# Performance work log

Measured on AMD Instinct MI355X. Metric: run time of the kernel, lower is better.

The kernel has to match this reference:

```python
import jax, jax.numpy as jnp
import numpy as np

HEADS, POINTS = 8, 4
EPS = 1e-5
BS, C, H, W = 2, 256, 200, 200


def _layernorm(x, g, b):
    m = x.mean(-1, keepdims=True)
    v = ((x - m) ** 2).mean(-1, keepdims=True)
    return (x - m) / jnp.sqrt(v + EPS) * g + b


def _sine_pos(bs, Hh, Ww, num_feats, temperature=10000.0):
    # mmdet SinePositionalEncoding with all-zeros mask: cumsum of ones -> 1..H / 1..W
    y = jnp.arange(1, Hh + 1, dtype=jnp.float32)
    x = jnp.arange(1, Ww + 1, dtype=jnp.float32)
    dim_t = jnp.arange(num_feats, dtype=jnp.float32)
    dim_t = temperature ** (2.0 * jnp.floor(dim_t / 2.0) / num_feats)

    def interleave(p):  # p: [N, num_feats] -> [sin(p0),cos(p1),sin(p2),...]
        return jnp.stack((jnp.sin(p[:, 0::2]), jnp.cos(p[:, 1::2])), axis=-1).reshape(p.shape[0], -1)

    pos_x = interleave(x[:, None] / dim_t)  # [W, nf]
    pos_y = interleave(y[:, None] / dim_t)  # [H, nf]
    pos = jnp.concatenate([
        jnp.broadcast_to(pos_y[:, None, :], (Hh, Ww, num_feats)),
        jnp.broadcast_to(pos_x[None, :, :], (Hh, Ww, num_feats)),
    ], axis=-1)  # [H, W, 2*nf] (channel order matches cat((pos_y,pos_x),dim=1) after flatten/permute)
    return jnp.broadcast_to(pos.reshape(1, Hh * Ww, 2 * num_feats), (bs, Hh * Ww, 2 * num_feats))


def _bilinear_sample(v, x, y):
    # v: [bs, heads, H, W, hd]; x, y: [bs, heads, N] pixel coords (align_corners=False, zero padding)
    bs, nh, Hh, Ww, hd = v.shape
    vf = v.reshape(bs, nh, Hh * Ww, hd)
    x0 = jnp.floor(x)
    y0 = jnp.floor(y)
    wx = x - x0
    wy = y - y0

    def gather(xi, yi):
        valid = (xi >= 0) & (xi < Ww) & (yi >= 0) & (yi < Hh)
        xc = jnp.clip(xi, 0, Ww - 1).astype(jnp.int32)
        yc = jnp.clip(yi, 0, Hh - 1).astype(jnp.int32)
        idx = yc * Ww + xc
        g = jnp.take_along_axis(vf, idx[..., None], axis=2)  # [bs, nh, N, hd]
        return g * valid[..., None].astype(v.dtype)

    out = gather(x0, y0) * ((1 - wx) * (1 - wy))[..., None]
    out = out + gather(x0 + 1, y0) * (wx * (1 - wy))[..., None]
    out = out + gather(x0, y0 + 1) * ((1 - wx) * wy)[..., None]
    out = out + gather(x0 + 1, y0 + 1) * (wx * wy)[..., None]
    return out


def _dfa_layer(out, ref, pos, Hh, Ww, p):
    bs, Lq, Cc = out.shape
    hd = Cc // HEADS
    q = out + pos
    value = out @ p['vp_w'].T + p['vp_b']  # [bs, Lq, C]
    off = (q @ p['off_w'].T + p['off_b']).reshape(bs, Lq, HEADS, POINTS, 2)
    aw = jax.nn.softmax((q @ p['aw_w'].T + p['aw_b']).reshape(bs, Lq, HEADS, POINTS), axis=-1)
    norm = jnp.array([Ww, Hh], dtype=out.dtype)
    loc = ref[None, :, None, None, :] + off / norm  # [bs, Lq, heads, P, 2] normalized [0,1]
    x = loc[..., 0] * Ww - 0.5
    y = loc[..., 1] * Hh - 0.5
    v = value.reshape(bs, Lq, HEADS, hd).transpose(0, 2, 1, 3).reshape(bs, HEADS, Hh, Ww, hd)
    xt = x.transpose(0, 2, 1, 3).reshape(bs, HEADS, Lq * POINTS)
    yt = y.transpose(0, 2, 1, 3).reshape(bs, HEADS, Lq * POINTS)
    samp = _bilinear_sample(v, xt, yt).reshape(bs, HEADS, Lq, POINTS, hd)
    attn = jnp.einsum('bhqpd,bqhp->bqhd', samp, aw).reshape(bs, Lq, Cc)
    attn = attn @ p['op_w'].T + p['op_b']
    out = _layernorm(out + attn, p['ln1_g'], p['ln1_b'])
    ffn = jax.nn.relu(out @ p['l1_w'].T + p['l1_b']) @ p['l2_w'].T + p['l2_b']
    return _layernorm(out + ffn, p['ln2_g'], p['ln2_b'])


def setup_inputs() -> dict:
    key = jax.random.key(0)
    ks = jax.random.split(key, 20)
    s = 0.02
    L = 3
    return {
        'bev_feat': jax.random.normal(ks[0], (BS, C, H, W), jnp.float32),
        'proj_q_w': jax.random.normal(ks[1], (C, C), jnp.float32) * s,
        'proj_q_b': jax.random.normal(ks[2], (C,), jnp.float32) * s,
        'off_w': jax.random.normal(ks[3], (L, HEADS * POINTS * 2, C), jnp.float32) * s,
        'off_b': jax.random.normal(ks[4], (L, HEADS * POINTS * 2), jnp.float32) * s,
        'aw_w': jax.random.normal(ks[5], (L, HEADS * POINTS, C), jnp.float32) * s,
        'aw_b': jax.random.normal(ks[6], (L, HEADS * POINTS), jnp.float32) * s,
        'vp_w': jax.random.normal(ks[7], (L, C, C), jnp.float32) * s,
        'vp_b': jax.random.normal(ks[8], (L, C), jnp.float32) * s,
        'op_w': jax.random.normal(ks[9], (L, C, C), jnp.float32) * s,
        'op_b': jax.random.normal(ks[10], (L, C), jnp.float32) * s,
        'ln1_g': jnp.ones((L, C), jnp.float32),
        'ln1_b': jnp.zeros((L, C), jnp.float32),
        'l1_w': jax.random.normal(ks[11], (L, C, C), jnp.float32) * s,
        'l1_b': jax.random.normal(ks[12], (L, C), jnp.float32) * s,
        'l2_w': jax.random.normal(ks[13], (L, C, C), jnp.float32) * s,
        'l2_b': jax.random.normal(ks[14], (L, C), jnp.float32) * s,
        'ln2_g': jnp.ones((L, C), jnp.float32),
        'ln2_b': jnp.zeros((L, C), jnp.float32),
    }


def reference(bev_feat, proj_q_w, proj_q_b, off_w, off_b, aw_w, aw_b, vp_w, vp_b,
              op_w, op_b, ln1_g, ln1_b, l1_w, l1_b, l2_w, l2_b, ln2_g, ln2_b):
    bs, Cc, Hh, Ww = bev_feat.shape
    x = bev_feat.reshape(bs, Cc, Hh * Ww).transpose(0, 2, 1)  # [bs, HW, C]
    out = x @ proj_q_w.T + proj_q_b
    # reference points: pixel centers normalized to [0,1]
    ry, rx = jnp.meshgrid(jnp.linspace(0.5, Hh - 0.5, Hh) / Hh,
                          jnp.linspace(0.5, Ww - 0.5, Ww) / Ww, indexing='ij')
    ref = jnp.stack([rx.reshape(-1), ry.reshape(-1)], axis=-1).astype(bev_feat.dtype)  # [HW, 2]
    pos = _sine_pos(bs, Hh, Ww, Cc // 2).astype(bev_feat.dtype)
    n_layers = off_w.shape[0]
    for i in range(n_layers):
        p = dict(off_w=off_w[i], off_b=off_b[i], aw_w=aw_w[i], aw_b=aw_b[i],
                 vp_w=vp_w[i], vp_b=vp_b[i], op_w=op_w[i], op_b=op_b[i],
                 ln1_g=ln1_g[i], ln1_b=ln1_b[i], l1_w=l1_w[i], l1_b=l1_b[i],
                 l2_w=l2_w[i], l2_b=l2_b[i], ln2_g=ln2_g[i], ln2_b=ln2_b[i])
        out = _dfa_layer(out, ref, pos, Hh, Ww, p)
    return out.transpose(0, 2, 1).reshape(bs, Cc, Hh, Ww)
```

## Files before the change

kernel.cpp:

```cpp
#include <hip/hip_runtime.h>
#include <math.h>

#define HEADS 8
#define POINTS 4
#define BSZ 2
#define CDIM 256
#define HH 200
#define WW 200
#define LQ (HH * WW)
#define MTOT (BSZ * LQ)
#define NLAYERS 3
#define MPAD 40064

typedef __attribute__((ext_vector_type(8))) short shortx8;
typedef __attribute__((ext_vector_type(4))) float floatx4;

__device__ __forceinline__ ushort f2b(float f) {
    union { float f; unsigned u; } v; v.f = f;
    unsigned r = v.u + 0x7fffu + ((v.u >> 16) & 1u);
    return (ushort)(r >> 16);
}
__device__ __forceinline__ float b2f(ushort b) {
    union { unsigned u; float f; } v; v.u = ((unsigned)b) << 16;
    return v.f;
}
__device__ __forceinline__ float bitsf(unsigned u) {
    union { unsigned u; float f; } v; v.u = u;
    return v.f;
}
__device__ __forceinline__ uint packbf(float lo, float hi) {
    return (uint)f2b(lo) | ((uint)f2b(hi) << 16);
}

__device__ __forceinline__ int permc(int c) {
    return (c & ~63) | (((c & 15) << 2) | ((c & 63) >> 4));
}
__device__ __forceinline__ int iperm(int p) {
    return (p & ~63) | (((p & 3) << 4) | ((p & 63) >> 2));
}

__global__ __launch_bounds__(256)
void cvt_kernel(const float* __restrict__ in, ushort* __restrict__ out)
{
    const int i = (blockIdx.x * 256 + threadIdx.x) * 4;
    const float4 v = *(const float4*)(in + i);
    ushort4 o;
    o.x = f2b(v.x); o.y = f2b(v.y); o.z = f2b(v.z); o.w = f2b(v.w);
    *(ushort4*)(out + i) = o;
}

__global__ __launch_bounds__(256)
void cvt_perm_kernel(const float* __restrict__ in, ushort* __restrict__ out)
{
    const int idx = (blockIdx.x * 256 + threadIdx.x) * 4;
    const int rowb = idx & ~255;
    const int p0 = idx & 255;
    ushort4 o;
    o.x = f2b(in[rowb + iperm(p0 + 0)]);
    o.y = f2b(in[rowb + iperm(p0 + 1)]);
    o.z = f2b(in[rowb + iperm(p0 + 2)]);
    o.w = f2b(in[rowb + iperm(p0 + 3)]);
    *(ushort4*)(out + idx) = o;
}

__global__ __launch_bounds__(256)
void build_offaw(const float* __restrict__ offw, const float* __restrict__ offb,
                 const float* __restrict__ aww, const float* __restrict__ awb,
                 ushort* __restrict__ wout, float* __restrict__ bout)
{
    const int blk = blockIdx.x;
    const int i = blk >> 7;
    const int r = blk & 127;
    const int c = threadIdx.x;
    float v = 0.f;
    if (r < 64)      v = offw[((size_t)i * 64 + r) * CDIM + c];
    else if (r < 96) v = aww[((size_t)i * 32 + (r - 64)) * CDIM + c];
    wout[((size_t)i * 128 + r) * CDIM + permc(c)] = f2b(v);
    if (c == 0) {
        float bb = 0.f;
        if (r < 64)      bb = offb[i * 64 + r];
        else if (r < 96) bb = awb[i * 32 + (r - 64)];
        bout[i * 128 + r] = bb;
    }
}

__global__ __launch_bounds__(256)
void pos_kernel(ushort* __restrict__ pos)
{
    const int idx = blockIdx.x * 256 + threadIdx.x;
    const int c = idx & 255;
    const int l = idx >> 8;
    const int cc = c & 127;
    const float coord = (c < 128) ? (float)(l / WW + 1) : (float)(l % WW + 1);
    const float expo = (float)(2 * (cc >> 1)) * (1.0f / 128.0f);
    const float t = powf(10000.0f, expo);
    const float ph = coord / t;
    pos[(size_t)l * CDIM + permc(c)] = f2b((cc & 1) ? cosf(ph) : sinf(ph));
}

__global__ __launch_bounds__(256)
void bevT_kernel(const float* __restrict__ in, ushort* __restrict__ out)
{
    __shared__ float tile[32][33];
    const int b = blockIdx.z;
    const int l0 = blockIdx.x * 32;
    const int c0 = blockIdx.y * 32;
    const float* ib = in + (size_t)b * CDIM * LQ;
    ushort* ob = out + (size_t)b * LQ * CDIM;
    #pragma unroll
    for (int j = 0; j < 32; j += 8)
        tile[threadIdx.y + j][threadIdx.x] =
            ib[(size_t)(c0 + threadIdx.y + j) * LQ + l0 + threadIdx.x];
    __syncthreads();
    #pragma unroll
    for (int j = 0; j < 32; j += 8)
        ob[(size_t)(l0 + threadIdx.y + j) * CDIM + c0 + threadIdx.x] =
            f2b(tile[threadIdx.x][threadIdx.y + j]);
}

#define LSTR 40

template<bool RELU, bool F32OUT, bool BF16OUT, bool ROWADD>
__global__ __launch_bounds__(256)
void mfma_gemm(const ushort* __restrict__ A, const ushort* __restrict__ B,
               const float* __restrict__ bias,
               float* __restrict__ Cf, ushort* __restrict__ Cb,
               const ushort* __restrict__ rowtab,
               int N, int K)
{
    __shared__ ushort As[128 * LSTR];
    __shared__ ushort Bs[128 * LSTR];
    const int tid = threadIdx.x;
    const int lane = tid & 63;
    const int wave = tid >> 6;
    const int wr = (wave >> 1) * 64;
    const int wc = (wave & 1) * 64;
    const int rowBase = blockIdx.y * 128;
    const int colBase = blockIdx.x * 128;

    floatx4 acc[4][4];
    #pragma unroll
    for (int i = 0; i < 4; i++)
        #pragma unroll
        for (int j = 0; j < 4; j++) {
            floatx4 z = {0.f, 0.f, 0.f, 0.f};
            acc[i][j] = z;
        }

    const int strow = tid >> 2;
    const int stcol = (tid & 3) * 8;
    const int kq = (lane >> 4) * 8;
    const int lr = lane & 15;

    for (int k0 = 0; k0 < K; k0 += 32) {
        #pragma unroll
        for (int j = 0; j < 2; j++) {
            const int r = j * 64 + strow;
            const uint4 av = *(const uint4*)(A + (size_t)(rowBase + r) * K + k0 + stcol);
            const uint4 bv = *(const uint4*)(B + (size_t)(colBase + r) * K + k0 + stcol);
            *(uint4*)(As + r * LSTR + stcol) = av;
            *(uint4*)(Bs + r * LSTR + stcol) = bv;
        }
        __syncthreads();
        shortx8 af[4], bfr[4];
        #pragma unroll
        for (int t = 0; t < 4; t++) {
            af[t]  = *(const shortx8*)(As + (wr + t * 16 + lr) * LSTR + kq);
            bfr[t] = *(const shortx8*)(Bs + (wc + t * 16 + lr) * LSTR + kq);
        }
        #pragma unroll
        for (int mt = 0; mt < 4; mt++)
            #pragma unroll
            for (int nt = 0; nt < 4; nt++)
                acc[mt][nt] = __builtin_amdgcn_mfma_f32_16x16x32_bf16(
                    af[mt], bfr[nt], acc[mt][nt], 0, 0, 0);
        __syncthreads();
    }

    const int colB = colBase + wc + lr;
    const int rowB = rowBase + wr + (lane >> 4) * 4;
    #pragma unroll
    for (int mt = 0; mt < 4; mt++) {
        #pragma unroll
        for (int r = 0; r < 4; r++) {
            const int m = rowB + mt * 16 + r;
            const int pr = (m >= LQ) ? m - LQ : m;
            #pragma unroll
            for (int nt = 0; nt < 4; nt++) {
                const int n = colB + nt * 16;
                float v = acc[mt][nt][r];
                if (ROWADD) v += b2f(rowtab[(size_t)pr * 384 + n]);
                else        v += bias[n];
                if (RELU) v = fmaxf(v, 0.f);
                if (F32OUT) Cf[(size_t)m * N + n] = v;
                if (BF16OUT) Cb[(size_t)m * N + n] = f2b(v);
            }
        }
    }
}

template<bool RELU, bool F32OUT, bool BF16OUT, bool PERMC>
__global__ __launch_bounds__(512, 1)
void gemm_fused(const ushort* __restrict__ A, const ushort* __restrict__ B,
                const float* __restrict__ bias,
                float* __restrict__ resid, ushort* __restrict__ Cb)
{
    __shared__ ushort As[2][128 * LSTR];
    __shared__ ushort Bs[2][256 * LSTR];

    const int tid = threadIdx.x;
    const int lane = tid & 63;
    const int wave = tid >> 6;
    const int lr = lane & 15;
    const int hi = lane >> 4;
    const int rowBase = blockIdx.x * 128;
    const int wr = (wave >> 2) * 64;
    const int wc = (wave & 3) * 64;

    floatx4 acc[4][4];
    #pragma unroll
    for (int i = 0; i < 4; i++)
        #pragma unroll
        for (int j = 0; j < 4; j++) {
            floatx4 z = {0.f, 0.f, 0.f, 0.f};
            acc[i][j] = z;
        }

    const int strow = tid >> 2;
    const int stcol = (tid & 3) * 8;
    const int kq = hi * 8;

    const ushort* ag = A + (size_t)(rowBase + strow) * CDIM + stcol;
    const ushort* bg = B + (size_t)strow * CDIM + stcol;

    {
        const uint4 av  = *(const uint4*)(ag);
        const uint4 bv0 = *(const uint4*)(bg);
        const uint4 bv1 = *(const uint4*)(bg + 128 * CDIM);
        *(uint4*)(As[0] + strow * LSTR + stcol) = av;
        *(uint4*)(Bs[0] + strow * LSTR + stcol) = bv0;
        *(uint4*)(Bs[0] + (strow + 128) * LSTR + stcol) = bv1;
    }

    #pragma unroll
    for (int kt = 0; kt < 8; ++kt) {
        const int p = kt & 1;
        __syncthreads();
        uint4 av, bv0, bv1;
        if (kt < 7) {
            const int ko = (kt + 1) * 32;
            av  = *(const uint4*)(ag + ko);
            bv0 = *(const uint4*)(bg + ko);
            bv1 = *(const uint4*)(bg + ko + 128 * CDIM);
        }
        shortx8 af[4], bfr[4];
        #pragma unroll
        for (int t = 0; t < 4; t++) {
            af[t]  = *(const shortx8*)(As[p] + (wr + t * 16 + lr) * LSTR + kq);
            bfr[t] = *(const shortx8*)(Bs[p] + (wc + t * 16 + lr) * LSTR + kq);
        }
        #pragma unroll
        for (int mt = 0; mt < 4; mt++)
            #pragma unroll
            for (int nt = 0; nt < 4; nt++)
                acc[mt][nt] = __builtin_amdgcn_mfma_f32_16x16x32_bf16(
                    af[mt], bfr[nt], acc[mt][nt], 0, 0, 0);
        if (kt < 7) {
            *(uint4*)(As[p ^ 1] + strow * LSTR + stcol) = av;
            *(uint4*)(Bs[p ^ 1] + strow * LSTR + stcol) = bv0;
            *(uint4*)(Bs[p ^ 1] + (strow + 128) * LSTR + stcol) = bv1;
        }
    }

    float bcol[4];
    #pragma unroll
    for (int nt = 0; nt < 4; nt++) bcol[nt] = bias[wc + nt * 16 + lr];

    #pragma unroll
    for (int mt = 0; mt < 4; mt++) {
        #pragma unroll
        for (int r = 0; r < 4; r++) {
            const int m = rowBase + wr + mt * 16 + hi * 4 + r;
            float4 wv;
            ushort4 ob;
            #pragma unroll
            for (int nt = 0; nt < 4; nt++) {
                float y = acc[mt][nt][r] + bcol[nt];
                if (RELU) y = fmaxf(y, 0.f);
                (&wv.x)[nt] = y;
                if (PERMC) {
                    if (BF16OUT) (&ob.x)[nt] = f2b(y);
                } else {
                    const int col = wc + nt * 16 + lr;
                    if (BF16OUT) Cb[(size_t)m * CDIM + col] = f2b(y);
                }
            }
            if (F32OUT) *(float4*)(resid + (size_t)m * CDIM + wc + lr * 4) = wv;
            if (PERMC && BF16OUT)
                *(ushort4*)(Cb + (size_t)m * CDIM + wc + lr * 4) = ob;
        }
    }
}

#define LSTR2 36
#define LSTR3 264

template<bool BF16OUT>
__global__ __launch_bounds__(256, 1)
void ffn_fused(const ushort* __restrict__ attn, const ushort* __restrict__ Wop,
               const float* __restrict__ opb,
               const ushort* __restrict__ Wl1, const float* __restrict__ l1b,
               const ushort* __restrict__ Wl2, const float* __restrict__ l2b,
               float* __restrict__ resid, ushort* __restrict__ outb,
               const float* __restrict__ g1, const float* __restrict__ b1,
               const float* __restrict__ g2, const float* __restrict__ b2)
{
    __shared__ ushort As[2][64 * LSTR2];
    __shared__ ushort Bs[2][256 * LSTR2];
    __shared__ ushort Ls[64 * LSTR3];

    const int tid = threadIdx.x;
    const int lane = tid & 63;
    const int wave = tid >> 6;
    const int lr = lane & 15;
    const int hi = lane >> 4;
    const int rowBase = blockIdx.x * 64;
    const int wc = wave * 64;

    const int strow = tid >> 2;
    const int stcol = (tid & 3) * 8;
    const int kq = hi * 8;

    floatx4 acc1[4][4];
    #pragma unroll
    for (int i = 0; i < 4; i++)
        #pragma unroll
        for (int j = 0; j < 4; j++) {
            floatx4 z = {0.f, 0.f, 0.f, 0.f};
            acc1[i][j] = z;
        }

    {
        const ushort* ag = attn + (size_t)(rowBase + strow) * CDIM + stcol;
        const ushort* bg = Wop + (size_t)strow * CDIM + stcol;
        {
            const uint4 av  = *(const uint4*)(ag);
            const uint4 bv0 = *(const uint4*)(bg);
            const uint4 bv1 = *(const uint4*)(bg + 64 * CDIM);
            const uint4 bv2 = *(const uint4*)(bg + 128 * CDIM);
            const uint4 bv3 = *(const uint4*)(bg + 192 * CDIM);
            *(uint4*)(As[0] + strow * LSTR2 + stcol) = av;
            *(uint4*)(Bs[0] + strow * LSTR2 + stcol) = bv0;
            *(uint4*)(Bs[0] + (strow + 64) * LSTR2 + stcol) = bv1;
            *(uint4*)(Bs[0] + (strow + 128) * LSTR2 + stcol) = bv2;
            *(uint4*)(Bs[0] + (strow + 192) * LSTR2 + stcol) = bv3;
        }
        #pragma unroll
        for (int kt = 0; kt < 8; ++kt) {
            const int p = kt & 1;
            __syncthreads();
            uint4 av, bv0, bv1, bv2, bv3;
            if (kt < 7) {
                const int ko = (kt + 1) * 32;
                av  = *(const uint4*)(ag + ko);
                bv0 = *(const uint4*)(bg + ko);
                bv1 = *(const uint4*)(bg + ko + 64 * CDIM);
                bv2 = *(const uint4*)(bg + ko + 128 * CDIM);
                bv3 = *(const uint4*)(bg + ko + 192 * CDIM);
            }
            shortx8 af[4], bfr[4];
            #pragma unroll
            for (int t = 0; t < 4; t++) {
                af[t]  = *(const shortx8*)(As[p] + (t * 16 + lr) * LSTR2 + kq);
                bfr[t] = *(const shortx8*)(Bs[p] + (wc + t * 16 + lr) * LSTR2 + kq);
            }
            #pragma unroll
            for (int mt = 0; mt < 4; mt++)
                #pragma unroll
                for (int nt = 0; nt < 4; nt++)
                    acc1[mt][nt] = __builtin_amdgcn_mfma_f32_16x16x32_bf16(
                        af[mt], bfr[nt], acc1[mt][nt], 0, 0, 0);
            if (kt < 7) {
                *(uint4*)(As[p ^ 1] + strow * LSTR2 + stcol) = av;
                *(uint4*)(Bs[p ^ 1] + strow * LSTR2 + stcol) = bv0;
                *(uint4*)(Bs[p ^ 1] + (strow + 64) * LSTR2 + stcol) = bv1;
                *(uint4*)(Bs[p ^ 1] + (strow + 128) * LSTR2 + stcol) = bv2;
                *(uint4*)(Bs[p ^ 1] + (strow + 192) * LSTR2 + stcol) = bv3;
            }
        }
        __syncthreads();
    }

    {
        float bcol[4];
        #pragma unroll
        for (int nt = 0; nt < 4; nt++) bcol[nt] = opb[wc + nt * 16 + lr];
        float2 (*red)[4] = (float2(*)[4])As[0];
        #pragma unroll
        for (int mt = 0; mt < 4; mt++) {
            #pragma unroll
            for (int r = 0; r < 4; r++) {
                const int mrel = mt * 16 + hi * 4 + r;
                const int m = rowBase + mrel;
                const float4 rv = *(const float4*)(resid + (size_t)m * CDIM + wc + lr * 4);
                float s = 0.f, sq = 0.f;
                #pragma unroll
                for (int nt = 0; nt < 4; nt++) {
                    float x = acc1[mt][nt][r] + bcol[nt] + (&rv.x)[nt];
                    acc1[mt][nt][r] = x;
                    s += x; sq += x * x;
                }
                #pragma unroll
                for (int o = 8; o >= 1; o >>= 1) {
                    s  += __shfl_xor(s, o, 64);
                    sq += __shfl_xor(sq, o, 64);
                }
                if (lr == 0) { float2 t2; t2.x = s; t2.y = sq; red[mrel][wave] = t2; }
            }
        }
        __syncthreads();
        float gcol[4], btcol[4];
        #pragma unroll
        for (int nt = 0; nt < 4; nt++) {
            gcol[nt]  = g1[wc + nt * 16 + lr];
            btcol[nt] = b1[wc + nt * 16 + lr];
        }
        #pragma unroll
        for (int mt = 0; mt < 4; mt++) {
            #pragma unroll
            for (int r = 0; r < 4; r++) {
                const int mrel = mt * 16 + hi * 4 + r;
                const float2 t0 = red[mrel][0], t1 = red[mrel][1];
                const float2 t2 = red[mrel][2], t3 = red[mrel][3];
                const float S  = (t0.x + t1.x) + (t2.x + t3.x);
                const float SQ = (t0.y + t1.y) + (t2.y + t3.y);
                const float mean = S * (1.0f / CDIM);
                const float var = SQ * (1.0f / CDIM) - mean * mean;
                const float rstd = rsqrtf(var + 1e-5f);
                ushort4 yb;
                #pragma unroll
                for (int nt = 0; nt < 4; nt++) {
                    const float y = (acc1[mt][nt][r] - mean) * rstd * gcol[nt] + btcol[nt];
                    acc1[mt][nt][r] = y;
                    (&yb.x)[nt] = f2b(y);
                }
                *(ushort4*)(Ls + mrel * LSTR3 + wc + lr * 4) = yb;
            }
        }
    }

    floatx4 acc2[4][4];
    #pragma unroll
    for (int i = 0; i < 4; i++)
        #pragma unroll
        for (int j = 0; j < 4; j++) {
            floatx4 z = {0.f, 0.f, 0.f, 0.f};
            acc2[i][j] = z;
        }
    {
        const ushort* bg = Wl1 + (size_t)strow * CDIM + stcol;
        {
            const uint4 bv0 = *(const uint4*)(bg);
            const uint4 bv1 = *(const uint4*)(bg + 64 * CDIM);
            const uint4 bv2 = *(const uint4*)(bg + 128 * CDIM);
            const uint4 bv3 = *(const uint4*)(bg + 192 * CDIM);
            *(uint4*)(Bs[0] + strow * LSTR2 + stcol) = bv0;
            *(uint4*)(Bs[0] + (strow + 64) * LSTR2 + stcol) = bv1;
            *(uint4*)(Bs[0] + (strow + 128) * LSTR2 + stcol) = bv2;
            *(uint4*)(Bs[0] + (strow + 192) * LSTR2 + stcol) = bv3;
        }
        #pragma unroll
        for (int kt = 0; kt < 8; ++kt) {
            const int p = kt & 1;
            __syncthreads();
            uint4 bv0, bv1, bv2, bv3;
            if (kt < 7) {
                const int ko = (kt + 1) * 32;
                bv0 = *(const uint4*)(bg + ko);
                bv1 = *(const uint4*)(bg + ko + 64 * CDIM);
                bv2 = *(const uint4*)(bg + ko + 128 * CDIM);
                bv3 = *(const uint4*)(bg + ko + 192 * CDIM);
            }
            shortx8 af[4], bfr[4];
            #pragma unroll
            for (int t = 0; t < 4; t++) {
                af[t]  = *(const shortx8*)(Ls + (t * 16 + lr) * LSTR3 + kt * 32 + kq);
                bfr[t] = *(const shortx8*)(Bs[p] + (wc + t * 16 + lr) * LSTR2 + kq);
            }
            #pragma unroll
            for (int mt = 0; mt < 4; mt++)
                #pragma unroll
                for (int nt = 0; nt < 4; nt++)
                    acc2[mt][nt] = __builtin_amdgcn_mfma_f32_16x16x32_bf16(
                        af[mt], bfr[nt], acc2[mt][nt], 0, 0, 0);
            if (kt < 7) {
                *(uint4*)(Bs[p ^ 1] + strow * LSTR2 + stcol) = bv0;
                *(uint4*)(Bs[p ^ 1] + (strow + 64) * LSTR2 + stcol) = bv1;
                *(uint4*)(Bs[p ^ 1] + (strow + 128) * LSTR2 + stcol) = bv2;
                *(uint4*)(Bs[p ^ 1] + (strow + 192) * LSTR2 + stcol) = bv3;
            }
        }
        __syncthreads();
        float bcol2[4];
        #pragma unroll
        for (int nt = 0; nt < 4; nt++) bcol2[nt] = l1b[wc + nt * 16 + lr];
        #pragma unroll
        for (int mt = 0; mt < 4; mt++) {
            #pragma unroll
            for (int r = 0; r < 4; r++) {
                const int mrel = mt * 16 + hi * 4 + r;
                ushort4 hb;
                #pragma unroll
                for (int nt = 0; nt < 4; nt++)
                    (&hb.x)[nt] = f2b(fmaxf(acc2[mt][nt][r] + bcol2[nt], 0.f));
                *(ushort4*)(Ls + mrel * LSTR3 + wc + lr * 4) = hb;
            }
        }
    }

    #pragma unroll
    for (int i = 0; i < 4; i++)
        #pragma unroll
        for (int j = 0; j < 4; j++) {
            floatx4 z = {0.f, 0.f, 0.f, 0.f};
            acc2[i][j] = z;
        }
    {
        const ushort* bg = Wl2 + (size_t)strow * CDIM + stcol;
        {
            const uint4 bv0 = *(const uint4*)(bg);
            const uint4 bv1 = *(const uint4*)(bg + 64 * CDIM);
            const uint4 bv2 = *(const uint4*)(bg + 128 * CDIM);
            const uint4 bv3 = *(const uint4*)(bg + 192 * CDIM);
            *(uint4*)(Bs[0] + strow * LSTR2 + stcol) = bv0;
            *(uint4*)(Bs[0] + (strow + 64) * LSTR2 + stcol) = bv1;
            *(uint4*)(Bs[0] + (strow + 128) * LSTR2 + stcol) = bv2;
            *(uint4*)(Bs[0] + (strow + 192) * LSTR2 + stcol) = bv3;
        }
        #pragma unroll
        for (int kt = 0; kt < 8; ++kt) {
            const int p = kt & 1;
            __syncthreads();
            uint4 bv0, bv1, bv2, bv3;
            if (kt < 7) {
                const int ko = (kt + 1) * 32;
                bv0 = *(const uint4*)(bg + ko);
                bv1 = *(const uint4*)(bg + ko + 64 * CDIM);
                bv2 = *(const uint4*)(bg + ko + 128 * CDIM);
                bv3 = *(const uint4*)(bg + ko + 192 * CDIM);
            }
            shortx8 af[4], bfr[4];
            #pragma unroll
            for (int t = 0; t < 4; t++) {
                af[t]  = *(const shortx8*)(Ls + (t * 16 + lr) * LSTR3 + kt * 32 + kq);
                bfr[t] = *(const shortx8*)(Bs[p] + (wc + t * 16 + lr) * LSTR2 + kq);
            }
            #pragma unroll
            for (int mt = 0; mt < 4; mt++)
                #pragma unroll
                for (int nt = 0; nt < 4; nt++)
                    acc2[mt][nt] = __builtin_amdgcn_mfma_f32_16x16x32_bf16(
                        af[mt], bfr[nt], acc2[mt][nt], 0, 0, 0);
            if (kt < 7) {
                *(uint4*)(Bs[p ^ 1] + strow * LSTR2 + stcol) = bv0;
                *(uint4*)(Bs[p ^ 1] + (strow + 64) * LSTR2 + stcol) = bv1;
                *(uint4*)(Bs[p ^ 1] + (strow + 128) * LSTR2 + stcol) = bv2;
                *(uint4*)(Bs[p ^ 1] + (strow + 192) * LSTR2 + stcol) = bv3;
            }
        }
        __syncthreads();
    }
    {
        float bcol3[4];
        #pragma unroll
        for (int nt = 0; nt < 4; nt++) bcol3[nt] = l2b[wc + nt * 16 + lr];
        float2 (*red)[4] = (float2(*)[4])As[0];
        #pragma unroll
        for (int mt = 0; mt < 4; mt++) {
            #pragma unroll
            for (int r = 0; r < 4; r++) {
                const int mrel = mt * 16 + hi * 4 + r;
                float s = 0.f, sq = 0.f;
                #pragma unroll
                for (int nt = 0; nt < 4; nt++) {
                    float x = acc2[mt][nt][r] + bcol3[nt] + acc1[mt][nt][r];
                    acc2[mt][nt][r] = x;
                    s += x; sq += x * x;
                }
                #pragma unroll
                for (int o = 8; o >= 1; o >>= 1) {
                    s  += __shfl_xor(s, o, 64);
                    sq += __shfl_xor(sq, o, 64);
                }
                if (lr == 0) { float2 t2; t2.x = s; t2.y = sq; red[mrel][wave] = t2; }
            }
        }
        __syncthreads();
        float gcol[4], btcol[4];
        #pragma unroll
        for (int nt = 0; nt < 4; nt++) {
            gcol[nt]  = g2[wc + nt * 16 + lr];
            btcol[nt] = b2[wc + nt * 16 + lr];
        }
        #pragma unroll
        for (int mt = 0; mt < 4; mt++) {
            #pragma unroll
            for (int r = 0; r < 4; r++) {
                const int mrel = mt * 16 + hi * 4 + r;
                const int m = rowBase + mrel;
                const float2 t0 = red[mrel][0], t1 = red[mrel][1];
                const float2 t2 = red[mrel][2], t3 = red[mrel][3];
                const float S  = (t0.x + t1.x) + (t2.x + t3.x);
                const float SQ = (t0.y + t1.y) + (t2.y + t3.y);
                const float mean = S * (1.0f / CDIM);
                const float var = SQ * (1.0f / CDIM) - mean * mean;
                const float rstd = rsqrtf(var + 1e-5f);
                float4 wv;
                ushort4 ob;
                #pragma unroll
                for (int nt = 0; nt < 4; nt++) {
                    const float y = (acc2[mt][nt][r] - mean) * rstd * gcol[nt] + btcol[nt];
                    (&wv.x)[nt] = y;
                    if (BF16OUT) (&ob.x)[nt] = f2b(y);
                }
                *(float4*)(resid + (size_t)m * CDIM + wc + lr * 4) = wv;
                if (BF16OUT) *(ushort4*)(outb + (size_t)m * CDIM + wc + lr * 4) = ob;
            }
        }
    }
}

__global__ __launch_bounds__(256)
void sample_kernel(const ushort* __restrict__ val,
                   const float* __restrict__ offaw,
                   ushort* __restrict__ attn)
{
    const int tid = threadIdx.x;
    const int m = blockIdx.x * 8 + (tid >> 5);
    const int lane = tid & 31;
    const int head = lane >> 2;
    const int c = head * 32 + (lane & 3) * 8;
    const int b = (m >= LQ) ? 1 : 0;
    const int l = m - (b ? LQ : 0);

    const float* row = offaw + (size_t)m * 128;
    const float4 lg  = *(const float4*)(row + 64 + head * 4);
    const float4 o01 = *(const float4*)(row + head * 8);
    const float4 o23 = *(const float4*)(row + head * 8 + 4);

    const float mx = fmaxf(fmaxf(lg.x, lg.y), fmaxf(lg.z, lg.w));
    const float e0 = expf(lg.x - mx), e1 = expf(lg.y - mx);
    const float e2 = expf(lg.z - mx), e3 = expf(lg.w - mx);
    const float inv = 1.0f / (e0 + e1 + e2 + e3);
    const float awv[4] = {e0 * inv, e1 * inv, e2 * inv, e3 * inv};

    const float lx = (float)(l % WW);
    const float ly = (float)(l / WW);
    const float px[4] = {lx + o01.x, lx + o01.z, lx + o23.x, lx + o23.z};
    const float py[4] = {ly + o01.y, ly + o01.w, ly + o23.y, ly + o23.w};

    const ushort* vb = val + (size_t)b * LQ * CDIM;
    uint4 cv[16];
    float cw[16];
    #pragma unroll
    for (int p = 0; p < POINTS; p++) {
        const float x = px[p], y = py[p];
        const float xf = floorf(x), yf = floorf(y);
        const int x0 = (int)xf, y0 = (int)yf;
        const float wx = x - xf, wy = y - yf;
        const int x0c = min(max(x0, 0), WW - 1);
        const int x1c = min(max(x0 + 1, 0), WW - 1);
        const int y0c = min(max(y0, 0), HH - 1);
        const int y1c = min(max(y0 + 1, 0), HH - 1);
        const float vx0 = (x0 >= 0 && x0 < WW) ? 1.f : 0.f;
        const float vx1 = (x0 + 1 >= 0 && x0 + 1 < WW) ? 1.f : 0.f;
        const float vy0 = (y0 >= 0 && y0 < HH) ? 1.f : 0.f;
        const float vy1 = (y0 + 1 >= 0 && y0 + 1 < HH) ? 1.f : 0.f;
        const float a = awv[p];
        cw[p * 4 + 0] = a * (1.f - wx) * (1.f - wy) * vx0 * vy0;
        cw[p * 4 + 1] = a * wx * (1.f - wy) * vx1 * vy0;
        cw[p * 4 + 2] = a * (1.f - wx) * wy * vx0 * vy1;
        cw[p * 4 + 3] = a * wx * wy * vx1 * vy1;
        const int r0 = y0c * WW, r1 = y1c * WW;
        cv[p * 4 + 0] = *(const uint4*)(vb + (((unsigned)(r0 + x0c)) << 8) + c);
        cv[p * 4 + 1] = *(const uint4*)(vb + (((unsigned)(r0 + x1c)) << 8) + c);
        cv[p * 4 + 2] = *(const uint4*)(vb + (((unsigned)(r1 + x0c)) << 8) + c);
        cv[p * 4 + 3] = *(const uint4*)(vb + (((unsigned)(r1 + x1c)) << 8) + c);
    }
    float a0 = 0.f, a1 = 0.f, a2 = 0.f, a3 = 0.f;
    float a4 = 0.f, a5 = 0.f, a6 = 0.f, a7 = 0.f;
    #pragma unroll
    for (int i = 0; i < 16; i++) {
        const float wgt = cw[i];
        a0 = fmaf(wgt, bitsf(cv[i].x << 16), a0);
        a1 = fmaf(wgt, bitsf(cv[i].x & 0xffff0000u), a1);
        a2 = fmaf(wgt, bitsf(cv[i].y << 16), a2);
        a3 = fmaf(wgt, bitsf(cv[i].y & 0xffff0000u), a3);
        a4 = fmaf(wgt, bitsf(cv[i].z << 16), a4);
        a5 = fmaf(wgt, bitsf(cv[i].z & 0xffff0000u), a5);
        a6 = fmaf(wgt, bitsf(cv[i].w << 16), a6);
        a7 = fmaf(wgt, bitsf(cv[i].w & 0xffff0000u), a7);
    }
    uint4 o;
    o.x = packbf(a0, a1); o.y = packbf(a2, a3);
    o.z = packbf(a4, a5); o.w = packbf(a6, a7);
    *(uint4*)(attn + (size_t)m * CDIM + c) = o;
}

__global__ __launch_bounds__(256)
void transpose_out(const float* __restrict__ in, float* __restrict__ outp)
{
    __shared__ float tile[32][33];
    const int b = blockIdx.z;
    const int l0 = blockIdx.x * 32;
    const int c0 = blockIdx.y * 32;
    const float* ib = in + (size_t)b * LQ * CDIM;
    float* ob = outp + (size_t)b * CDIM * LQ;
    #pragma unroll
    for (int j = 0; j < 32; j += 8)
        tile[threadIdx.y + j][threadIdx.x] =
            ib[(size_t)(l0 + threadIdx.y + j) * CDIM + c0 + threadIdx.x];
    __syncthreads();
    #pragma unroll
    for (int j = 0; j < 32; j += 8)
        ob[(size_t)iperm(c0 + threadIdx.y + j) * LQ + l0 + threadIdx.x] =
            tile[threadIdx.x][threadIdx.y + j];
}

extern "C" void kernel_launch(void* const* d_in, const int* in_sizes, int n_in,
                              void* d_out, int out_size, void* d_ws, size_t ws_size,
                              hipStream_t stream)
{
    const float* bev      = (const float*)d_in[0];
    const float* proj_q_w = (const float*)d_in[1];
    const float* proj_q_b = (const float*)d_in[2];
    const float* off_w    = (const float*)d_in[3];
    const float* off_b    = (const float*)d_in[4];
    const float* aw_w     = (const float*)d_in[5];
    const float* aw_b     = (const float*)d_in[6];
    const float* vp_w     = (const float*)d_in[7];
    const float* vp_b     = (const float*)d_in[8];
    const float* op_w     = (const float*)d_in[9];
    const float* op_b     = (const float*)d_in[10];
    const float* ln1_g    = (const float*)d_in[11];
    const float* ln1_b    = (const float*)d_in[12];
    const float* l1_w     = (const float*)d_in[13];
    const float* l1_b     = (const float*)d_in[14];
    const float* l2_w     = (const float*)d_in[15];
    const float* l2_b     = (const float*)d_in[16];
    const float* ln2_g    = (const float*)d_in[17];
    const float* ln2_b    = (const float*)d_in[18];
    float* outp = (float*)d_out;

    char* w = (char*)d_ws;
    float*  out_f    = (float*)(w);
    float*  offaw_f  = (float*)(w + 81920000);
    ushort* attn_b   = (ushort*)(w + 122880000);
    ushort* out_b    = (ushort*)(w + 163840000);
    ushort* posoff_b = (ushort*)(w + 204800000);
    ushort* val_b    = (ushort*)(w + 245760000);
    ushort* pos_b    = (ushort*)(w + 286720000);
    ushort* w_b      = (ushort*)(w + 307200000);
    ushort* wproj = w_b;
    ushort* wvp   = w_b + 65536;
    ushort* wop   = w_b + 65536 + 196608;
    ushort* wl1   = w_b + 65536 + 2 * 196608;
    ushort* wl2   = w_b + 65536 + 3 * 196608;
    ushort* wofa  = w_b + 65536 + 4 * 196608;
    float*  bofa  = (float*)(w + 307200000 + 2 * (65536 + 4 * 196608 + 98304));

    const dim3 blk(256);
    const dim3 blk512(512);

    cvt_kernel<<<dim3(65536 / 1024), blk, 0, stream>>>(proj_q_w, wproj);
    cvt_perm_kernel<<<dim3(196608 / 1024), blk, 0, stream>>>(vp_w, wvp);
    cvt_kernel<<<dim3(196608 / 1024), blk, 0, stream>>>(op_w, wop);
    cvt_perm_kernel<<<dim3(196608 / 1024), blk, 0, stream>>>(l1_w, wl1);
    cvt_perm_kernel<<<dim3(196608 / 1024), blk, 0, stream>>>(l2_w, wl2);
    build_offaw<<<dim3(3 * 128), blk, 0, stream>>>(off_w, off_b, aw_w, aw_b, wofa, bofa);
    pos_kernel<<<dim3((LQ * CDIM) / 256), blk, 0, stream>>>(pos_b);
    bevT_kernel<<<dim3(LQ / 32, CDIM / 32, BSZ), dim3(32, 8), 0, stream>>>(bev, val_b);

    mfma_gemm<false, false, true, false><<<dim3(3, MPAD / 128), blk, 0, stream>>>(
        pos_b, wofa, bofa, nullptr, posoff_b, nullptr, 384, CDIM);

    const dim3 gF(MTOT / 128);
    const dim3 gFFN(MTOT / 64);
    const dim3 g128(1, MTOT / 128);

    gemm_fused<false, true, true, true><<<gF, blk512, 0, stream>>>(
        val_b, wproj, proj_q_b, out_f, out_b);

    for (int i = 0; i < NLAYERS; i++) {
        gemm_fused<false, false, true, false><<<gF, blk512, 0, stream>>>(
            out_b, wvp + (size_t)i * 65536, vp_b + (size_t)i * CDIM,
            nullptr, val_b);
        mfma_gemm<false, true, false, true><<<g128, blk, 0, stream>>>(
            out_b, wofa + (size_t)i * 32768, nullptr,
            offaw_f, nullptr, posoff_b + (size_t)i * 128, 128, CDIM);
        sample_kernel<<<dim3(MTOT / 8), blk, 0, stream>>>(val_b, offaw_f, attn_b);
        if (i < NLAYERS - 1) {
            ffn_fused<true><<<gFFN, blk, 0, stream>>>(
                attn_b, wop + (size_t)i * 65536, op_b + (size_t)i * CDIM,
                wl1 + (size_t)i * 65536, l1_b + (size_t)i * CDIM,
                wl2 + (size_t)i * 65536, l2_b + (size_t)i * CDIM,
                out_f, out_b,
                ln1_g + (size_t)i * CDIM, ln1_b + (size_t)i * CDIM,
                ln2_g + (size_t)i * CDIM, ln2_b + (size_t)i * CDIM);
        } else {
            ffn_fused<false><<<gFFN, blk, 0, stream>>>(
                attn_b, wop + (size_t)i * 65536, op_b + (size_t)i * CDIM,
                wl1 + (size_t)i * 65536, l1_b + (size_t)i * CDIM,
                wl2 + (size_t)i * 65536, l2_b + (size_t)i * CDIM,
                out_f, nullptr,
                ln1_g + (size_t)i * CDIM, ln1_b + (size_t)i * CDIM,
                ln2_g + (size_t)i * CDIM, ln2_b + (size_t)i * CDIM);
        }
    }

    transpose_out<<<dim3(LQ / 32, CDIM / 32, BSZ), dim3(32, 8), 0, stream>>>(out_f, outp);
}
```

Measured before the change: 1.038 ms.

## Replace double-buffered LDS staging with single buffer in fused FFN kernel

Removes the register-prefetch double buffering in the three GEMM stages of the fused FFN kernel. Each k-step now loads from global, stores to a single LDS buffer, syncs, computes, and syncs again. This halves the As/Bs shared memory footprint and lowers register pressure, which may allow more resident blocks. In exchange, global load latency is no longer hidden behind the MFMA work and each step pays an extra barrier.

Result: no change. 1.050 ms (+1.1%).

```diff
diff --git a/kernel.cpp b/kernel.cpp
--- a/kernel.cpp
+++ b/kernel.cpp
@@ -315,8 +315,8 @@
                const float* __restrict__ g1, const float* __restrict__ b1,
                const float* __restrict__ g2, const float* __restrict__ b2)
 {
-    __shared__ ushort As[2][64 * LSTR2];
-    __shared__ ushort Bs[2][256 * LSTR2];
+    __shared__ ushort As[64 * LSTR2];
+    __shared__ ushort Bs[256 * LSTR2];
     __shared__ ushort Ls[64 * LSTR3];
 
     const int tid = threadIdx.x;
@@ -343,36 +343,25 @@
     {
         const ushort* ag = attn + (size_t)(rowBase + strow) * CDIM + stcol;
         const ushort* bg = Wop + (size_t)strow * CDIM + stcol;
-        {
-            const uint4 av  = *(const uint4*)(ag);
-            const uint4 bv0 = *(const uint4*)(bg);
-            const uint4 bv1 = *(const uint4*)(bg + 64 * CDIM);
-            const uint4 bv2 = *(const uint4*)(bg + 128 * CDIM);
-            const uint4 bv3 = *(const uint4*)(bg + 192 * CDIM);
-            *(uint4*)(As[0] + strow * LSTR2 + stcol) = av;
-            *(uint4*)(Bs[0] + strow * LSTR2 + stcol) = bv0;
-            *(uint4*)(Bs[0] + (strow + 64) * LSTR2 + stcol) = bv1;
-            *(uint4*)(Bs[0] + (strow + 128) * LSTR2 + stcol) = bv2;
-            *(uint4*)(Bs[0] + (strow + 192) * LSTR2 + stcol) = bv3;
-        }
         #pragma unroll
         for (int kt = 0; kt < 8; ++kt) {
-            const int p = kt & 1;
+            const int ko = kt * 32;
+            const uint4 av  = *(const uint4*)(ag + ko);
+            const uint4 bv0 = *(const uint4*)(bg + ko);
+            const uint4 bv1 = *(const uint4*)(bg + ko + 64 * CDIM);
+            const uint4 bv2 = *(const uint4*)(bg + ko + 128 * CDIM);
+            const uint4 bv3 = *(const uint4*)(bg + ko + 192 * CDIM);
+            *(uint4*)(As + strow * LSTR2 + stcol) = av;
+            *(uint4*)(Bs + strow * LSTR2 + stcol) = bv0;
+            *(uint4*)(Bs + (strow + 64) * LSTR2 + stcol) = bv1;
+            *(uint4*)(Bs + (strow + 128) * LSTR2 + stcol) = bv2;
+            *(uint4*)(Bs + (strow + 192) * LSTR2 + stcol) = bv3;
             __syncthreads();
-            uint4 av, bv0, bv1, bv2, bv3;
-            if (kt < 7) {
-                const int ko = (kt + 1) * 32;
-                av  = *(const uint4*)(ag + ko);
-                bv0 = *(const uint4*)(bg + ko);
-                bv1 = *(const uint4*)(bg + ko + 64 * CDIM);
-                bv2 = *(const uint4*)(bg + ko + 128 * CDIM);
-                bv3 = *(const uint4*)(bg + ko + 192 * CDIM);
-            }
             shortx8 af[4], bfr[4];
             #pragma unroll
             for (int t = 0; t < 4; t++) {
-                af[t]  = *(const shortx8*)(As[p] + (t * 16 + lr) * LSTR2 + kq);
-                bfr[t] = *(const shortx8*)(Bs[p] + (wc + t * 16 + lr) * LSTR2 + kq);
+                af[t]  = *(const shortx8*)(As + (t * 16 + lr) * LSTR2 + kq);
+                bfr[t] = *(const shortx8*)(Bs + (wc + t * 16 + lr) * LSTR2 + kq);
             }
             #pragma unroll
             for (int mt = 0; mt < 4; mt++)
@@ -380,22 +369,15 @@
                 for (int nt = 0; nt < 4; nt++)
                     acc1[mt][nt] = __builtin_amdgcn_mfma_f32_16x16x32_bf16(
                         af[mt], bfr[nt], acc1[mt][nt], 0, 0, 0);
-            if (kt < 7) {
-                *(uint4*)(As[p ^ 1] + strow * LSTR2 + stcol) = av;
-                *(uint4*)(Bs[p ^ 1] + strow * LSTR2 + stcol) = bv0;
-                *(uint4*)(Bs[p ^ 1] + (strow + 64) * LSTR2 + stcol) = bv1;
-                *(uint4*)(Bs[p ^ 1] + (strow + 128) * LSTR2 + stcol) = bv2;
-                *(uint4*)(Bs[p ^ 1] + (strow + 192) * LSTR2 + stcol) = bv3;
-            }
-        }
-        __syncthreads();
+            __syncthreads();
+        }
     }
 
     {
         float bcol[4];
         #pragma unroll
         for (int nt = 0; nt < 4; nt++) bcol[nt] = opb[wc + nt * 16 + lr];
-        float2 (*red)[4] = (float2(*)[4])As[0];
+        float2 (*red)[4] = (float2(*)[4])As;
         #pragma unroll
         for (int mt = 0; mt < 4; mt++) {
             #pragma unroll
@@ -459,33 +441,23 @@
         }
     {
         const ushort* bg = Wl1 + (size_t)strow * CDIM + stcol;
-        {
-            const uint4 bv0 = *(const uint4*)(bg);
-            const uint4 bv1 = *(const uint4*)(bg + 64 * CDIM);
-            const uint4 bv2 = *(const uint4*)(bg + 128 * CDIM);
-            const uint4 bv3 = *(const uint4*)(bg + 192 * CDIM);
-            *(uint4*)(Bs[0] + strow * LSTR2 + stcol) = bv0;
-            *(uint4*)(Bs[0] + (strow + 64) * LSTR2 + stcol) = bv1;
-            *(uint4*)(Bs[0] + (strow + 128) * LSTR2 + stcol) = bv2;
-            *(uint4*)(Bs[0] + (strow + 192) * LSTR2 + stcol) = bv3;
-        }
         #pragma unroll
         for (int kt = 0; kt < 8; ++kt) {
-            const int p = kt & 1;
+            const int ko = kt * 32;
+            const uint4 bv0 = *(const uint4*)(bg + ko);
+            const uint4 bv1 = *(const uint4*)(bg + ko + 64 * CDIM);
+            const uint4 bv2 = *(const uint4*)(bg + ko + 128 * CDIM);
+            const uint4 bv3 = *(const uint4*)(bg + ko + 192 * CDIM);
+            *(uint4*)(Bs + strow * LSTR2 + stcol) = bv0;
+            *(uint4*)(Bs + (strow + 64) * LSTR2 + stcol) = bv1;
+            *(uint4*)(Bs + (strow + 128) * LSTR2 + stcol) = bv2;
+            *(uint4*)(Bs + (strow + 192) * LSTR2 + stcol) = bv3;
             __syncthreads();
-            uint4 bv0, bv1, bv2, bv3;
-            if (kt < 7) {
-                const int ko = (kt + 1) * 32;
-                bv0 = *(const uint4*)(bg + ko);
-                bv1 = *(const uint4*)(bg + ko + 64 * CDIM);
-                bv2 = *(const uint4*)(bg + ko + 128 * CDIM);
-                bv3 = *(const uint4*)(bg + ko + 192 * CDIM);
-            }
             shortx8 af[4], bfr[4];
             #pragma unroll
             for (int t = 0; t < 4; t++) {
-                af[t]  = *(const shortx8*)(Ls + (t * 16 + lr) * LSTR3 + kt * 32 + kq);
-                bfr[t] = *(const shortx8*)(Bs[p] + (wc + t * 16 + lr) * LSTR2 + kq);
+                af[t]  = *(const shortx8*)(Ls + (t * 16 + lr) * LSTR3 + ko + kq);
+                bfr[t] = *(const shortx8*)(Bs + (wc + t * 16 + lr) * LSTR2 + kq);
             }
             #pragma unroll
             for (int mt = 0; mt < 4; mt++)
@@ -493,14 +465,8 @@
                 for (int nt = 0; nt < 4; nt++)
                     acc2[mt][nt] = __builtin_amdgcn_mfma_f32_16x16x32_bf16(
                         af[mt], bfr[nt], acc2[mt][nt], 0, 0, 0);
-            if (kt < 7) {
-                *(uint4*)(Bs[p ^ 1] + strow * LSTR2 + stcol) = bv0;
-                *(uint4*)(Bs[p ^ 1] + (strow + 64) * LSTR2 + stcol) = bv1;
-                *(uint4*)(Bs[p ^ 1] + (strow + 128) * LSTR2 + stcol) = bv2;
-                *(uint4*)(Bs[p ^ 1] + (strow + 192) * LSTR2 + stcol) = bv3;
-            }
-        }
-        __syncthreads();
+            __syncthreads();
+        }
         float bcol2[4];
         #pragma unroll
         for (int nt = 0; nt < 4; nt++) bcol2[nt] = l1b[wc + nt * 16 + lr];
@@ -527,33 +493,23 @@
         }
     {
         const ushort* bg = Wl2 + (size_t)strow * CDIM + stcol;
-        {
-            const uint4 bv0 = *(const uint4*)(bg);
-            const uint4 bv1 = *(const uint4*)(bg + 64 * CDIM);
-            const uint4 bv2 = *(const uint4*)(bg + 128 * CDIM);
-            const uint4 bv3 = *(const uint4*)(bg + 192 * CDIM);
-            *(uint4*)(Bs[0] + strow * LSTR2 + stcol) = bv0;
-            *(uint4*)(Bs[0] + (strow + 64) * LSTR2 + stcol) = bv1;
-            *(uint4*)(Bs[0] + (strow + 128) * LSTR2 + stcol) = bv2;
-            *(uint4*)(Bs[0] + (strow + 192) * LSTR2 + stcol) = bv3;
-        }
         #pragma unroll
         for (int kt = 0; kt < 8; ++kt) {
-            const int p = kt & 1;
+            const int ko = kt * 32;
+            const uint4 bv0 = *(const uint4*)(bg + ko);
+            const uint4 bv1 = *(const uint4*)(bg + ko + 64 * CDIM);
+            const uint4 bv2 = *(const uint4*)(bg + ko + 128 * CDIM);
+            const uint4 bv3 = *(const uint4*)(bg + ko + 192 * CDIM);
+            *(uint4*)(Bs + strow * LSTR2 + stcol) = bv0;
+            *(uint4*)(Bs + (strow + 64) * LSTR2 + stcol) = bv1;
+            *(uint4*)(Bs + (strow + 128) * LSTR2 + stcol) = bv2;
+            *(uint4*)(Bs + (strow + 192) * LSTR2 + stcol) = bv3;
             __syncthreads();
-            uint4 bv0, bv1, bv2, bv3;
-            if (kt < 7) {
-                const int ko = (kt + 1) * 32;
-                bv0 = *(const uint4*)(bg + ko);
-                bv1 = *(const uint4*)(bg + ko + 64 * CDIM);
-                bv2 = *(const uint4*)(bg + ko + 128 * CDIM);
-                bv3 = *(const uint4*)(bg + ko + 192 * CDIM);
-            }
             shortx8 af[4], bfr[4];
             #pragma unroll
             for (int t = 0; t < 4; t++) {
-                af[t]  = *(const shortx8*)(Ls + (t * 16 + lr) * LSTR3 + kt * 32 + kq);
-                bfr[t] = *(const shortx8*)(Bs[p] + (wc + t * 16 + lr) * LSTR2 + kq);
+                af[t]  = *(const shortx8*)(Ls + (t * 16 + lr) * LSTR3 + ko + kq);
+                bfr[t] = *(const shortx8*)(Bs + (wc + t * 16 + lr) * LSTR2 + kq);
             }
             #pragma unroll
             for (int mt = 0; mt < 4; mt++)
@@ -561,20 +517,14 @@
                 for (int nt = 0; nt < 4; nt++)
                     acc2[mt][nt] = __builtin_amdgcn_mfma_f32_16x16x32_bf16(
                         af[mt], bfr[nt], acc2[mt][nt], 0, 0, 0);
-            if (kt < 7) {
-                *(uint4*)(Bs[p ^ 1] + strow * LSTR2 + stcol) = bv0;
-                *(uint4*)(Bs[p ^ 1] + (strow + 64) * LSTR2 + stcol) = bv1;
-                *(uint4*)(Bs[p ^ 1] + (strow + 128) * LSTR2 + stcol) = bv2;
-                *(uint4*)(Bs[p ^ 1] + (strow + 192) * LSTR2 + stcol) = bv3;
-            }
-        }
-        __syncthreads();
+            __syncthreads();
+        }
     }
     {
         float bcol3[4];
         #pragma unroll
         for (int nt = 0; nt < 4; nt++) bcol3[nt] = l2b[wc + nt * 16 + lr];
-        float2 (*red)[4] = (float2(*)[4])As[0];
+        float2 (*red)[4] = (float2(*)[4])As;
         #pragma unroll
         for (int mt = 0; mt < 4; mt++) {
             #pragma unroll
```
